# Kernel tuning notes

Hardware: AMD Instinct MI355X
Metric: run time of the kernel (lower is better)

## Reference

```python
import jax, jax.numpy as jnp
import numpy as np

S = (128, 128, 128)  # spatial grid
K = (16, 16, 16)     # retained low-frequency modes


def _gelu(x):
    # torch nn.GELU default = exact erf variant
    return jax.nn.gelu(x, approximate=False)


def _flayer(x, Rr, Ri, w):
    # x: (s1,s2,s3,dv). Full rfftn then truncate to low modes (as in source).
    f = jnp.fft.rfftn(x, axes=(0, 1, 2))[: K[0], : K[1], : K[2]]  # (k1,k2,k3,dv) complex
    Rf = jnp.einsum('abcd,abcde->abce', f, Rr + 1j * Ri)           # per-mode channel mix
    kernelpart = jnp.fft.irfftn(Rf, s=S, axes=(0, 1, 2))           # zero-pad modes, back to grid
    return _gelu(kernelpart + x @ w)


def setup_inputs() -> dict:
    key = jax.random.key(0)
    ks = jax.random.split(key, 20)
    da, dv, dout = 4, 32, 1
    sc1, sc2, sc3 = 2.0 / da, 2.0 / dv, 2.0 / dv
    d = {}
    d['x'] = jax.random.normal(ks[0], (*S, da), dtype=jnp.float32)
    d['win'] = sc1 * jax.random.normal(ks[1], (da, dv), dtype=jnp.float32)
    d['bin1'] = sc1 * jax.random.normal(ks[2], (dv,), dtype=jnp.float32)
    i = 3
    for L in range(1, 5):
        d[f'Rphir{L}'] = sc2 * jax.random.normal(ks[i], (*K, dv, dv), dtype=jnp.float32); i += 1
        d[f'Rphii{L}'] = sc2 * jax.random.normal(ks[i], (*K, dv, dv), dtype=jnp.float32); i += 1
        d[f'w{L}'] = sc2 * jax.random.normal(ks[i], (dv, dv), dtype=jnp.float32); i += 1
    d['wout'] = sc3 * jax.random.normal(ks[i], (dv, dout), dtype=jnp.float32); i += 1
    d['bout'] = sc3 * jax.random.normal(ks[i], (dout,), dtype=jnp.float32)
    return d


def reference(x, win, bin1, Rphir1, Rphii1, w1, Rphir2, Rphii2, w2,
              Rphir3, Rphii3, w3, Rphir4, Rphii4, w4, wout, bout):
    v = _gelu(x @ win + bin1)          # lifting: (s1,s2,s3,dv)
    v = _flayer(v, Rphir1, Rphii1, w1)
    v = _flayer(v, Rphir2, Rphii2, w2)
    v = _flayer(v, Rphir3, Rphii3, w3)
    v = _flayer(v, Rphir4, Rphii4, w4)
    return v @ wout + bout             # (s1,s2,s3,dout)
```

## Files before the change

### kernel.cpp

```cpp
#include <hip/hip_runtime.h>
#include <math.h>

typedef float2 cplx;
typedef _Float16 h16;
typedef h16 h16x8 __attribute__((ext_vector_type(8)));
typedef float f32x4 __attribute__((ext_vector_type(4)));
typedef uint u32x2 __attribute__((ext_vector_type(2)));

#define MFMA16(a, b, c) __builtin_amdgcn_mfma_f32_16x16x32_f16(a, b, c, 0, 0, 0)

static __device__ __forceinline__ float gelu_exact(float z) {
  float x = z * 0.70710678118654752440f;
  float ax = fabsf(x);
  float t = __builtin_amdgcn_rcpf(fmaf(0.3275911f, ax, 1.0f));
  float p = fmaf(1.061405429f, t, -1.453152027f);
  p = fmaf(p, t, 1.421413741f);
  p = fmaf(p, t, -0.284496736f);
  p = fmaf(p, t, 0.254829592f);
  p = p * t;
  float e = __expf(-ax * ax);
  float erfax = fmaf(-p, e, 1.0f);
  float er = copysignf(erfax, x);
  return 0.5f * z * (1.0f + er);
}

template <int OFF>
static __device__ __forceinline__ h16x8 tr_frag(uint addr) {
  union { uint u[4]; h16x8 h; } r;
  u32x2 lo, hi;
  asm volatile("ds_read_b64_tr_b16 %0, %2 offset:%3\n\t"
               "ds_read_b64_tr_b16 %1, %2 offset:%4"
               : "=&v"(lo), "=&v"(hi)
               : "v"(addr), "i"(OFF), "i"(OFF + 128));
  r.u[0] = lo.x; r.u[1] = lo.y; r.u[2] = hi.x; r.u[3] = hi.y;
  return r.h;
}

__global__ __launch_bounds__(256) void k_prep(
    h16* __restrict__ Afwd, h16* __restrict__ Adt, cplx* __restrict__ Twc,
    const float* __restrict__ wA, const float* __restrict__ wB,
    const float* __restrict__ wC, const float* __restrict__ wD,
    h16* __restrict__ Wfr)
{
  const int tid = threadIdx.x;
  const float w0 = 0.049087385212340519f;
  for (int idx = tid; idx < 4096; idx += 256) {
    int Mt = idx >> 11, rem = idx & 2047, lane = rem >> 5, k = rem & 31;
    int j = k & 7, chunk = k >> 3;
    int m = lane & 15;
    int x3 = chunk * 32 + (lane >> 4) * 8 + j;
    float ang = (float)((m * x3) & 127) * w0;
    float s, c; sincosf(ang, &s, &c);
    float val = Mt ? s : c;
    h16 hi = (h16)val;
    Afwd[idx] = hi;
    Afwd[idx + 4096] = (h16)(val - (float)hi);
  }
  for (int idx = tid; idx < 4096; idx += 256) {
    int tt = idx >> 4, rem = idx & 15, t = rem >> 3, j = rem & 7;
    int wv = tt >> 6, lane = tt & 63, mrow = lane & 15, q = lane >> 4;
    int x3 = (2 * wv + t) * 16 + mrow;
    int kk = q * 8 + j;
    int m = (kk < 16) ? kk : kk - 16;
    float ang = (float)((x3 * m) & 127) * w0;
    float s, c; sincosf(ang, &s, &c);
    Adt[idx] = (h16)((kk < 16) ? c : s);
  }
  const float* ws[4] = { wA, wB, wC, wD };
  for (int idx = tid; idx < 16384; idx += 256) {
    int L = idx >> 12, rem = idx & 4095;
    int t2 = rem >> 4, nt = (rem >> 3) & 1, j = rem & 7;
    int mrow = t2 & 15, q = (t2 >> 4) & 3;
    int n = nt * 16 + mrow, kk = q * 8 + j;
    Wfr[idx] = (h16)ws[L][kk * 32 + n];
  }
  if (tid < 128) {
    float ang = (float)tid * w0;
    float s, c; sincosf(ang, &s, &c);
    Twc[tid] = make_float2(c, s);
  }
}

__global__ __launch_bounds__(256) void k_lift(
    const float* __restrict__ x, const float* __restrict__ win,
    const float* __restrict__ bin, h16* __restrict__ v)
{
  __shared__ float xr[512];
  __shared__ float wl[128];
  __shared__ float bl[32];
  const int tid = threadIdx.x;
  const size_t b = blockIdx.x;
  const float* xrow = x + b * 512;
  for (int i = tid; i < 512; i += 256) xr[i] = xrow[i];
  if (tid < 128) wl[tid] = win[tid];
  if (tid < 32)  bl[tid] = bin[tid];
  __syncthreads();
  const int c = tid & 31, g = tid >> 5;
  #pragma unroll
  for (int j = 0; j < 16; ++j) {
    int x3 = g + 8 * j;
    float z = bl[c];
    #pragma unroll
    for (int a = 0; a < 4; ++a) z += xr[x3 * 4 + a] * wl[a * 32 + c];
    v[b * 4096 + x3 * 32 + c] = (h16)gelu_exact(z);
  }
}

__global__ __launch_bounds__(256) void k_fwd3(
    const h16* __restrict__ v, const h16* __restrict__ Afwd, cplx* __restrict__ Gp,
    const cplx* __restrict__ twg)
{
  __shared__ __align__(16) h16 vtile[4][2][4][32][16];
  __shared__ cplx F3L[4][512];
  __shared__ cplx twc[128];
  const int tid = threadIdx.x;
  const int x1 = blockIdx.x, qs = blockIdx.y;
  if (tid < 128) twc[tid] = twg[tid];
  const int lane = tid & 63, wv = tid >> 6;
  const int mrow = lane & 15, q4 = lane >> 4;
  h16x8 Ah[2][4], Al[2][4];
  #pragma unroll
  for (int Mt = 0; Mt < 2; ++Mt)
    #pragma unroll
    for (int ch = 0; ch < 4; ++ch) {
      Ah[Mt][ch] = *(const h16x8*)&Afwd[Mt * 2048 + lane * 32 + ch * 8];
      Al[Mt][ch] = *(const h16x8*)&Afwd[4096 + Mt * 2048 + lane * 32 + ch * 8];
    }
  const uint ldsbase = (uint)(uintptr_t)&vtile[0][0][0][0][0];
  const uint abase = ldsbase + (uint)(wv * 8192 + q4 * 256 + mrow * 2);
  cplx g0[16], g1[16];
  #pragma unroll
  for (int k2 = 0; k2 < 16; ++k2) { g0[k2] = make_float2(0.f, 0.f); g1[k2] = make_float2(0.f, 0.f); }
  for (int it = 0; it < 8; ++it) {
    const int x2b = qs * 32 + it * 4;
    __syncthreads();
    const uint4* vsrc = (const uint4*)(v + ((size_t)x1 * 128 + x2b) * 4096);
    for (int i = tid; i < 2048; i += 256) {
      uint4 pk = vsrc[i];
      int rr = i >> 9, e = (i & 511) * 8, x3 = e >> 5, c0 = e & 31;
      int panel = c0 >> 4, off = c0 & 15;
      int chunk = x3 >> 5, row = x3 & 31;
      *(uint4*)&vtile[rr][panel][chunk][row][off] = pk;
    }
    __syncthreads();
    h16x8 B0[4], B1[4];
    {
      const uint a0 = abase;
      const uint a1 = abase + 4096;
      B0[0] = tr_frag<0>(a0);    B0[1] = tr_frag<1024>(a0);
      B0[2] = tr_frag<2048>(a0); B0[3] = tr_frag<3072>(a0);
      B1[0] = tr_frag<0>(a1);    B1[1] = tr_frag<1024>(a1);
      B1[2] = tr_frag<2048>(a1); B1[3] = tr_frag<3072>(a1);
      asm volatile("s_waitcnt lgkmcnt(0)" ::: "memory");
      __builtin_amdgcn_sched_barrier(0);
    }
    f32x4 acc[2][2];
    #pragma unroll
    for (int Mt = 0; Mt < 2; ++Mt)
      #pragma unroll
      for (int Nt = 0; Nt < 2; ++Nt) acc[Mt][Nt] = (f32x4){0.f, 0.f, 0.f, 0.f};
    #pragma unroll
    for (int ch = 0; ch < 4; ++ch) {
      acc[0][0] = MFMA16(Ah[0][ch], B0[ch], acc[0][0]);
      acc[0][0] = MFMA16(Al[0][ch], B0[ch], acc[0][0]);
      acc[0][1] = MFMA16(Ah[0][ch], B1[ch], acc[0][1]);
      acc[0][1] = MFMA16(Al[0][ch], B1[ch], acc[0][1]);
      acc[1][0] = MFMA16(Ah[1][ch], B0[ch], acc[1][0]);
      acc[1][0] = MFMA16(Al[1][ch], B0[ch], acc[1][0]);
      acc[1][1] = MFMA16(Ah[1][ch], B1[ch], acc[1][1]);
      acc[1][1] = MFMA16(Al[1][ch], B1[ch], acc[1][1]);
    }
    #pragma unroll
    for (int Nt = 0; Nt < 2; ++Nt)
      #pragma unroll
      for (int r = 0; r < 4; ++r)
        F3L[wv][(q4 * 4 + r) * 32 + Nt * 16 + mrow] =
            make_float2(acc[0][Nt][r], -acc[1][Nt][r]);
    __syncthreads();
    #pragma unroll
    for (int rr = 0; rr < 4; ++rr) {
      const int x2 = x2b + rr;
      cplx f0 = F3L[rr][tid], f1 = F3L[rr][tid + 256];
      #pragma unroll
      for (int k2 = 0; k2 < 16; ++k2) {
        cplx t = twc[(k2 * x2) & 127];
        g0[k2].x += f0.x * t.x + f0.y * t.y;  g0[k2].y += f0.y * t.x - f0.x * t.y;
        g1[k2].x += f1.x * t.x + f1.y * t.y;  g1[k2].y += f1.y * t.x - f1.x * t.y;
      }
    }
  }
  cplx* dst = Gp + (size_t)qs * 1048576;
  #pragma unroll
  for (int k2 = 0; k2 < 16; ++k2) {
    size_t base = ((size_t)x1 * 16 + k2) * 512;
    dst[base + tid] = g0[k2];
    dst[base + 256 + tid] = g1[k2];
  }
}

__global__ __launch_bounds__(256) void k_spec(
    const cplx* __restrict__ Gp, const float* __restrict__ Rr,
    const float* __restrict__ Ri, cplx* __restrict__ H1,
    const cplx* __restrict__ twg)
{
  __shared__ cplx twc[128];
  __shared__ cplx fb[512];
  __shared__ cplx tb[512];
  const int tid = threadIdx.x;
  const int k2 = blockIdx.x >> 4, k3 = blockIdx.x & 15;
  if (tid < 128) twc[tid] = twg[tid];
  __syncthreads();
  const int c = tid & 31, g = tid >> 5;
  float fr0 = 0.f, fi0 = 0.f, fr1 = 0.f, fi1 = 0.f;
  #pragma unroll 4
  for (int x1 = 0; x1 < 128; ++x1) {
    size_t idx = (((size_t)x1 * 16 + k2) * 16 + k3) * 32 + c;
    cplx p0 = Gp[idx], p1 = Gp[idx + 1048576], p2 = Gp[idx + 2097152], p3 = Gp[idx + 3145728];
    cplx h = make_float2(p0.x + p1.x + p2.x + p3.x, p0.y + p1.y + p2.y + p3.y);
    cplx ta = twc[(g * x1) & 127];
    cplx tb2 = twc[((g + 8) * x1) & 127];
    fr0 += h.x * ta.x + h.y * ta.y;   fi0 += h.y * ta.x - h.x * ta.y;
    fr1 += h.x * tb2.x + h.y * tb2.y; fi1 += h.y * tb2.x - h.x * tb2.y;
  }
  fb[g * 32 + c] = make_float2(fr0, fi0);
  fb[(g + 8) * 32 + c] = make_float2(fr1, fi1);
  __syncthreads();
  {
    const int e = c;
    float tr0 = 0.f, ti0 = 0.f, tr1 = 0.f, ti1 = 0.f;
    const size_t mb0 = ((size_t)g * 256 + k2 * 16 + k3) * 1024;
    const size_t mb1 = ((size_t)(g + 8) * 256 + k2 * 16 + k3) * 1024;
    #pragma unroll 4
    for (int cc = 0; cc < 32; ++cc) {
      float rr0 = Rr[mb0 + cc * 32 + e], ri0 = Ri[mb0 + cc * 32 + e];
      float rr1 = Rr[mb1 + cc * 32 + e], ri1 = Ri[mb1 + cc * 32 + e];
      cplx f0 = fb[g * 32 + cc], f1 = fb[(g + 8) * 32 + cc];
      tr0 += f0.x * rr0 - f0.y * ri0;  ti0 += f0.x * ri0 + f0.y * rr0;
      tr1 += f1.x * rr1 - f1.y * ri1;  ti1 += f1.x * ri1 + f1.y * rr1;
    }
    const float s = 4.76837158203125e-07f;
    tb[g * 32 + e] = make_float2(tr0 * s, ti0 * s);
    tb[(g + 8) * 32 + e] = make_float2(tr1 * s, ti1 * s);
  }
  __syncthreads();
  float trr[16], tii[16];
  #pragma unroll
  for (int k1 = 0; k1 < 16; ++k1) { cplx t = tb[k1 * 32 + c]; trr[k1] = t.x; tii[k1] = t.y; }
  #pragma unroll
  for (int j = 0; j < 16; ++j) {
    int xx1 = g + 8 * j;
    float hr = 0.f, hi = 0.f;
    #pragma unroll
    for (int k1 = 0; k1 < 16; ++k1) {
      cplx t = twc[(k1 * xx1) & 127];
      hr += trr[k1] * t.x - tii[k1] * t.y;
      hi += trr[k1] * t.y + tii[k1] * t.x;
    }
    H1[(((size_t)xx1 * 16 + k2) * 16 + k3) * 32 + c] = make_float2(hr, hi);
  }
}

__global__ __launch_bounds__(512) void k_ptm3(
    const cplx* __restrict__ H1, const h16* __restrict__ Wfr,
    h16* __restrict__ v, const h16* __restrict__ Adt,
    const cplx* __restrict__ twg)
{
  __shared__ __align__(16) h16 St[2][32 * 40];
  const int tid = threadIdx.x;
  const int x1 = blockIdx.y;
  const int x2b = blockIdx.x * 8;
  const int c = tid & 31, g2 = (tid >> 5) & 15;
  const int lane = tid & 63, w = tid >> 6;
  const int mrow = lane & 15, q = lane >> 4;
  h16x8 Adf, Bw[2];
  Adf   = *(const h16x8*)&Adt[((w >> 1) * 64 + lane) * 16 + (w & 1) * 8];
  Bw[0] = *(const h16x8*)&Wfr[lane * 16];
  Bw[1] = *(const h16x8*)&Wfr[lane * 16 + 8];
  cplx h1[16];
  {
    const cplx* h1p = H1 + (size_t)x1 * 8192;
    #pragma unroll
    for (int k2 = 0; k2 < 16; ++k2) h1[k2] = h1p[(k2 * 16 + g2) * 32 + c];
  }
  const float s0 = (g2 == 0) ? 1.f : 2.f;
  for (int xi = 0; xi < 8; ++xi) {
    const int x2 = x2b + xi;
    const size_t b = (size_t)x1 * 128 + x2;
    h16x8 Av = *(const h16x8*)&v[b * 4096 + (w * 16 + mrow) * 32 + q * 8];
    float r = 0.f, i = 0.f;
    #pragma unroll
    for (int k2 = 0; k2 < 16; ++k2) {
      cplx t = twg[(k2 * x2) & 127];
      r += h1[k2].x * t.x - h1[k2].y * t.y;
      i += h1[k2].x * t.y + h1[k2].y * t.x;
    }
    h16* stp = St[xi & 1];
    stp[c * 40 + g2]      = (h16)(s0 * r);
    stp[c * 40 + 16 + g2] = (h16)(-s0 * i);
    __syncthreads();
    f32x4 acc[2];
    #pragma unroll
    for (int nt = 0; nt < 2; ++nt) {
      h16x8 Bst = *(const h16x8*)&stp[(nt * 16 + mrow) * 40 + q * 8];
      f32x4 z = {0.f, 0.f, 0.f, 0.f};
      z = MFMA16(Adf, Bst, z);
      z = MFMA16(Av, Bw[nt], z);
      acc[nt] = z;
    }
    #pragma unroll
    for (int nt = 0; nt < 2; ++nt)
      #pragma unroll
      for (int r2 = 0; r2 < 4; ++r2) {
        int x3 = w * 16 + q * 4 + r2;
        v[b * 4096 + x3 * 32 + nt * 16 + mrow] = (h16)gelu_exact(acc[nt][r2]);
      }
  }
}

__global__ __launch_bounds__(512) void k_ptf3(
    const cplx* __restrict__ H1, const h16* __restrict__ Wfr,
    const h16* __restrict__ v, const h16* __restrict__ Adt,
    const float* __restrict__ wout, const float* __restrict__ bout,
    float* __restrict__ out, const cplx* __restrict__ twg)
{
  __shared__ __align__(16) h16 St[2][32 * 40];
  const int tid = threadIdx.x;
  const int x1 = blockIdx.y;
  const int x2b = blockIdx.x * 8;
  const int c = tid & 31, g2 = (tid >> 5) & 15;
  const int lane = tid & 63, w = tid >> 6;
  const int mrow = lane & 15, q = lane >> 4;
  h16x8 Adf, Bw[2];
  Adf   = *(const h16x8*)&Adt[((w >> 1) * 64 + lane) * 16 + (w & 1) * 8];
  Bw[0] = *(const h16x8*)&Wfr[lane * 16];
  Bw[1] = *(const h16x8*)&Wfr[lane * 16 + 8];
  const float wo0 = wout[mrow], wo1 = wout[16 + mrow];
  const float bo = bout[0];
  cplx h1[16];
  {
    const cplx* h1p = H1 + (size_t)x1 * 8192;
    #pragma unroll
    for (int k2 = 0; k2 < 16; ++k2) h1[k2] = h1p[(k2 * 16 + g2) * 32 + c];
  }
  const float s0 = (g2 == 0) ? 1.f : 2.f;
  for (int xi = 0; xi < 8; ++xi) {
    const int x2 = x2b + xi;
    const size_t b = (size_t)x1 * 128 + x2;
    h16x8 Av = *(const h16x8*)&v[b * 4096 + (w * 16 + mrow) * 32 + q * 8];
    float r = 0.f, i = 0.f;
    #pragma unroll
    for (int k2 = 0; k2 < 16; ++k2) {
      cplx t = twg[(k2 * x2) & 127];
      r += h1[k2].x * t.x - h1[k2].y * t.y;
      i += h1[k2].x * t.y + h1[k2].y * t.x;
    }
    h16* stp = St[xi & 1];
    stp[c * 40 + g2]      = (h16)(s0 * r);
    stp[c * 40 + 16 + g2] = (h16)(-s0 * i);
    __syncthreads();
    f32x4 acc[2];
    #pragma unroll
    for (int nt = 0; nt < 2; ++nt) {
      h16x8 Bst = *(const h16x8*)&stp[(nt * 16 + mrow) * 40 + q * 8];
      f32x4 z = {0.f, 0.f, 0.f, 0.f};
      z = MFMA16(Adf, Bst, z);
      z = MFMA16(Av, Bw[nt], z);
      acc[nt] = z;
    }
    #pragma unroll
    for (int r2 = 0; r2 < 4; ++r2) {
      float p = (float)(h16)gelu_exact(acc[0][r2]) * wo0
              + (float)(h16)gelu_exact(acc[1][r2]) * wo1;
      p += __shfl_xor(p, 1);
      p += __shfl_xor(p, 2);
      p += __shfl_xor(p, 4);
      p += __shfl_xor(p, 8);
      if (mrow == 0) {
        int x3 = w * 16 + q * 4 + r2;
        out[b * 128 + x3] = bo + p;
      }
    }
  }
}

__global__ void k_diag(float* out, float wsmb) {
  if (threadIdx.x == 0 && blockIdx.x == 0) out[0] = wsmb;
}

extern "C" void kernel_launch(void* const* d_in, const int* in_sizes, int n_in,
                              void* d_out, int out_size, void* d_ws, size_t ws_size,
                              hipStream_t stream)
{
  (void)in_sizes; (void)n_in; (void)out_size;
  const float* x    = (const float*)d_in[0];
  const float* win  = (const float*)d_in[1];
  const float* bin1 = (const float*)d_in[2];
  const float* Rr[4] = { (const float*)d_in[3], (const float*)d_in[6],
                         (const float*)d_in[9], (const float*)d_in[12] };
  const float* Ri[4] = { (const float*)d_in[4], (const float*)d_in[7],
                         (const float*)d_in[10], (const float*)d_in[13] };
  const float* wm[4] = { (const float*)d_in[5], (const float*)d_in[8],
                         (const float*)d_in[11], (const float*)d_in[14] };
  const float* wout = (const float*)d_in[15];
  const float* bout = (const float*)d_in[16];
  float* out = (float*)d_out;

  const size_t SZ_V  = 134217728;
  const size_t SZ_C  = 33554432;
  const size_t SZ_AF = 16384;
  const size_t SZ_AD = 8192;
  const size_t SZ_TW = 1024;
  const size_t SZ_WF = 32768;
  const size_t NEED = SZ_V + SZ_C + SZ_AF + SZ_AD + SZ_TW + SZ_WF;

  if (ws_size < NEED) {
    k_diag<<<1, 64, 0, stream>>>(out, (float)(ws_size >> 20));
    return;
  }
  char* p = (char*)d_ws;
  h16* v    = (h16*)p;  p += SZ_V;
  cplx* C   = (cplx*)p; p += SZ_C;
  h16* Afwd = (h16*)p;  p += SZ_AF;
  h16* Adt  = (h16*)p;  p += SZ_AD;
  cplx* Twc = (cplx*)p; p += SZ_TW;
  h16* Wfr  = (h16*)p;

  k_prep<<<1, 256, 0, stream>>>(Afwd, Adt, Twc, wm[0], wm[1], wm[2], wm[3], Wfr);
  k_lift<<<16384, 256, 0, stream>>>(x, win, bin1, v);
  for (int L = 0; L < 4; ++L) {
    k_fwd3<<<dim3(128, 4), 256, 0, stream>>>(v, Afwd, C, Twc);
    k_spec<<<256, 256, 0, stream>>>(C, Rr[L], Ri[L], C, Twc);
    if (L < 3) k_ptm3<<<dim3(16, 128), 512, 0, stream>>>(C, Wfr + (size_t)L * 4096, v, Adt, Twc);
    else       k_ptf3<<<dim3(16, 128), 512, 0, stream>>>(C, Wfr + 3 * 4096, v, Adt, wout, bout, out, Twc);
  }
}
```

Baseline: 825.9 us.

## Split spectral kernel x1 reduction across two half-blocks and read twiddles from global

k_spec becomes k_spec2 with 512 threads per block. Each half of the block reduces over 64 of the 128 x1 values and the two partials are summed in LDS. This doubles per-block parallelism for the latency-bound x1 DFT and for the per-mode channel mix. Separately, k_fwd3 drops its LDS twiddle copy and reads twiddles directly from global/cache, trading LDS reads and one sync for cached global loads.

```diff
diff --git a/kernel.cpp b/kernel.cpp
--- a/kernel.cpp
+++ b/kernel.cpp
@@ -112,10 +112,8 @@
 {
   __shared__ __align__(16) h16 vtile[4][2][4][32][16];
   __shared__ cplx F3L[4][512];
-  __shared__ cplx twc[128];
   const int tid = threadIdx.x;
   const int x1 = blockIdx.x, qs = blockIdx.y;
-  if (tid < 128) twc[tid] = twg[tid];
   const int lane = tid & 63, wv = tid >> 6;
   const int mrow = lane & 15, q4 = lane >> 4;
   h16x8 Ah[2][4], Al[2][4];
@@ -183,7 +181,7 @@
       cplx f0 = F3L[rr][tid], f1 = F3L[rr][tid + 256];
       #pragma unroll
       for (int k2 = 0; k2 < 16; ++k2) {
-        cplx t = twc[(k2 * x2) & 127];
+        cplx t = twg[(k2 * x2) & 127];
         g0[k2].x += f0.x * t.x + f0.y * t.y;  g0[k2].y += f0.y * t.x - f0.x * t.y;
         g1[k2].x += f1.x * t.x + f1.y * t.y;  g1[k2].y += f1.y * t.x - f1.x * t.y;
       }
@@ -198,57 +196,59 @@
   }
 }
 
-__global__ __launch_bounds__(256) void k_spec(
+__global__ __launch_bounds__(512) void k_spec2(
     const cplx* __restrict__ Gp, const float* __restrict__ Rr,
     const float* __restrict__ Ri, cplx* __restrict__ H1,
     const cplx* __restrict__ twg)
 {
   __shared__ cplx twc[128];
-  __shared__ cplx fb[512];
+  __shared__ cplx fbp[2][512];
   __shared__ cplx tb[512];
   const int tid = threadIdx.x;
   const int k2 = blockIdx.x >> 4, k3 = blockIdx.x & 15;
   if (tid < 128) twc[tid] = twg[tid];
   __syncthreads();
-  const int c = tid & 31, g = tid >> 5;
+  const int c = tid & 31, g = (tid >> 5) & 7, h = tid >> 8;
   float fr0 = 0.f, fi0 = 0.f, fr1 = 0.f, fi1 = 0.f;
   #pragma unroll 4
-  for (int x1 = 0; x1 < 128; ++x1) {
+  for (int x1i = 0; x1i < 64; ++x1i) {
+    const int x1 = h * 64 + x1i;
     size_t idx = (((size_t)x1 * 16 + k2) * 16 + k3) * 32 + c;
     cplx p0 = Gp[idx], p1 = Gp[idx + 1048576], p2 = Gp[idx + 2097152], p3 = Gp[idx + 3145728];
-    cplx h = make_float2(p0.x + p1.x + p2.x + p3.x, p0.y + p1.y + p2.y + p3.y);
+    cplx hh = make_float2(p0.x + p1.x + p2.x + p3.x, p0.y + p1.y + p2.y + p3.y);
     cplx ta = twc[(g * x1) & 127];
     cplx tb2 = twc[((g + 8) * x1) & 127];
-    fr0 += h.x * ta.x + h.y * ta.y;   fi0 += h.y * ta.x - h.x * ta.y;
-    fr1 += h.x * tb2.x + h.y * tb2.y; fi1 += h.y * tb2.x - h.x * tb2.y;
-  }
-  fb[g * 32 + c] = make_float2(fr0, fi0);
-  fb[(g + 8) * 32 + c] = make_float2(fr1, fi1);
+    fr0 += hh.x * ta.x + hh.y * ta.y;   fi0 += hh.y * ta.x - hh.x * ta.y;
+    fr1 += hh.x * tb2.x + hh.y * tb2.y; fi1 += hh.y * tb2.x - hh.x * tb2.y;
+  }
+  fbp[h][g * 32 + c] = make_float2(fr0, fi0);
+  fbp[h][(g + 8) * 32 + c] = make_float2(fr1, fi1);
   __syncthreads();
   {
-    const int e = c;
-    float tr0 = 0.f, ti0 = 0.f, tr1 = 0.f, ti1 = 0.f;
-    const size_t mb0 = ((size_t)g * 256 + k2 * 16 + k3) * 1024;
-    const size_t mb1 = ((size_t)(g + 8) * 256 + k2 * 16 + k3) * 1024;
+    cplx a = fbp[0][tid], b = fbp[1][tid];
+    fbp[0][tid] = make_float2(a.x + b.x, a.y + b.y);
+  }
+  __syncthreads();
+  {
+    const int k1 = tid >> 5, e = c;
+    float tr = 0.f, ti = 0.f;
+    const size_t mb = ((size_t)k1 * 256 + k2 * 16 + k3) * 1024;
     #pragma unroll 4
     for (int cc = 0; cc < 32; ++cc) {
-      float rr0 = Rr[mb0 + cc * 32 + e], ri0 = Ri[mb0 + cc * 32 + e];
-      float rr1 = Rr[mb1 + cc * 32 + e], ri1 = Ri[mb1 + cc * 32 + e];
-      cplx f0 = fb[g * 32 + cc], f1 = fb[(g + 8) * 32 + cc];
-      tr0 += f0.x * rr0 - f0.y * ri0;  ti0 += f0.x * ri0 + f0.y * rr0;
-      tr1 += f1.x * rr1 - f1.y * ri1;  ti1 += f1.x * ri1 + f1.y * rr1;
+      float rr0 = Rr[mb + cc * 32 + e], ri0 = Ri[mb + cc * 32 + e];
+      cplx f0 = fbp[0][k1 * 32 + cc];
+      tr += f0.x * rr0 - f0.y * ri0;  ti += f0.x * ri0 + f0.y * rr0;
     }
     const float s = 4.76837158203125e-07f;
-    tb[g * 32 + e] = make_float2(tr0 * s, ti0 * s);
-    tb[(g + 8) * 32 + e] = make_float2(tr1 * s, ti1 * s);
+    tb[k1 * 32 + e] = make_float2(tr * s, ti * s);
   }
   __syncthreads();
   float trr[16], tii[16];
   #pragma unroll
   for (int k1 = 0; k1 < 16; ++k1) { cplx t = tb[k1 * 32 + c]; trr[k1] = t.x; tii[k1] = t.y; }
   #pragma unroll
-  for (int j = 0; j < 16; ++j) {
-    int xx1 = g + 8 * j;
+  for (int jj = 0; jj < 8; ++jj) {
+    int xx1 = g + 64 * h + 8 * jj;
     float hr = 0.f, hi = 0.f;
     #pragma unroll
     for (int k1 = 0; k1 < 16; ++k1) {
@@ -429,7 +429,7 @@
   k_lift<<<16384, 256, 0, stream>>>(x, win, bin1, v);
   for (int L = 0; L < 4; ++L) {
     k_fwd3<<<dim3(128, 4), 256, 0, stream>>>(v, Afwd, C, Twc);
-    k_spec<<<256, 256, 0, stream>>>(C, Rr[L], Ri[L], C, Twc);
+    k_spec2<<<256, 512, 0, stream>>>(C, Rr[L], Ri[L], C, Twc);
     if (L < 3) k_ptm3<<<dim3(16, 128), 512, 0, stream>>>(C, Wfr + (size_t)L * 4096, v, Adt, Twc);
     else       k_ptf3<<<dim3(16, 128), 512, 0, stream>>>(C, Wfr + 3 * 4096, v, Adt, wout, bout, out, Twc);
   }
```

Measured after the change: 768.5 us. 7.0% less time.
